# Kernel tuning notes

Measured on AMD Instinct MI355X. Metric: run time of the kernel, lower is better.

## Reference

```python
import math
import jax, jax.numpy as jnp
import numpy as np

B, N, DIM, H, DH = 2, 1024, 1024, 16, 64
SCALE = 16.0  # cosine_sim_scale
LN_EPS = 1e-5


def layer_norm(x, g, eps=LN_EPS):
    # torch: unbiased=False variance
    m = jnp.mean(x, axis=-1, keepdims=True)
    v = jnp.var(x, axis=-1, keepdims=True)
    return (x - m) * jax.lax.rsqrt(v + eps) * g


def l2norm(t):
    # F.normalize(dim=-1): x / max(||x||, 1e-12)
    n = jnp.linalg.norm(t, axis=-1, keepdims=True)
    return t / jnp.maximum(n, 1e-12)


def setup_inputs() -> dict:
    key = jax.random.key(0)
    ks = jax.random.split(key, 8)
    x = jax.random.normal(ks[0], (B, N, DIM), jnp.float32)
    attn_bias = jax.random.normal(ks[1], (B, H, N, N + 1), jnp.float32) * 0.02
    g_in = jnp.ones((DIM,), jnp.float32)
    w_q = jax.random.normal(ks[2], (H * DH, DIM), jnp.float32) * 0.02
    w_kv = jax.random.normal(ks[3], (2 * DH, DIM), jnp.float32) * 0.02
    null_kv = jax.random.normal(ks[4], (2, DH), jnp.float32)
    w_out = jax.random.normal(ks[5], (DIM, H * DH), jnp.float32) * 0.02
    g_out = jnp.ones((DIM,), jnp.float32)
    mask = jnp.ones((B, N), dtype=bool)
    return dict(x=x, attn_bias=attn_bias, g_in=g_in, w_q=w_q, w_kv=w_kv,
                null_kv=null_kv, w_out=w_out, g_out=g_out, mask=mask)


def reference(x, attn_bias, g_in, w_q, w_kv, null_kv, w_out, g_out, mask):
    b, n, _ = x.shape
    xn = layer_norm(x, g_in)
    q = xn @ w_q.T                      # [b, n, H*DH]
    kv = xn @ w_kv.T                    # [b, n, 2*DH]  (single kv head)
    k, v = kv[..., :DH], kv[..., DH:]
    q = q.reshape(b, n, H, DH).transpose(0, 2, 1, 3) * SCALE  # [b, h, n, d]
    nk = jnp.broadcast_to(null_kv[0], (b, 1, DH))
    nv = jnp.broadcast_to(null_kv[1], (b, 1, DH))
    k = jnp.concatenate([nk, k], axis=1)  # [b, n+1, d]
    v = jnp.concatenate([nv, v], axis=1)
    # cosine-sim attention: l2norm then scale by sqrt(cosine_sim_scale)
    q = l2norm(q) * math.sqrt(SCALE)
    k = l2norm(k) * math.sqrt(SCALE)
    sim = jnp.einsum('bhid,bjd->bhij', q, k) + attn_bias
    mask_p = jnp.concatenate([jnp.ones((b, 1), dtype=bool), mask], axis=1)  # null kv always visible
    max_neg = -jnp.finfo(sim.dtype).max
    sim = jnp.where(mask_p[:, None, None, :], sim, max_neg)
    attn = jax.nn.softmax(sim.astype(jnp.float32), axis=-1).astype(sim.dtype)
    out = jnp.einsum('bhij,bjd->bhid', attn, v)
    out = out.transpose(0, 2, 1, 3).reshape(b, n, H * DH)
    out = out @ w_out.T
    return layer_norm(out, g_out)
```

## Files before the change

kernel.cpp:

```cpp
#include <hip/hip_runtime.h>
#include <math.h>

#define B_   2
#define N_   1024
#define DIM_ 1024
#define H_   16
#define NK_  1025
#define NKP_ 1088
#define LOG2E 1.4426950408889634f

typedef __attribute__((ext_vector_type(8))) short s16x8;
typedef __attribute__((ext_vector_type(4))) float f32x4;

__device__ __forceinline__ float wave_sum(float v) {
  #pragma unroll
  for (int off = 32; off; off >>= 1) v += __shfl_xor(v, off);
  return v;
}
__device__ __forceinline__ short f2bf(float f) {
  union { float f; unsigned u; } v; v.f = f;
  unsigned r = (v.u + 0x7fffu + ((v.u >> 16) & 1u)) >> 16;
  return (short)r;
}
__device__ __forceinline__ float bf2f(short s) {
  union { unsigned u; float f; } v; v.u = ((unsigned)(unsigned short)s) << 16;
  return v.f;
}
__device__ __forceinline__ void gl_lds16(const void* g, void* lds) {
  __builtin_amdgcn_global_load_lds(
      (const __attribute__((address_space(1))) void*)g,
      (__attribute__((address_space(3))) void*)lds, 16, 0, 0);
}
__device__ __forceinline__ void gl_lds4(const void* g, void* lds) {
  __builtin_amdgcn_global_load_lds(
      (const __attribute__((address_space(1))) void*)g,
      (__attribute__((address_space(3))) void*)lds, 4, 0, 0);
}

__device__ __forceinline__ size_t kf_idx(int b, int j, int d) {
  return (((size_t)b * 68 + (j >> 4)) * 2 + (d >> 5)) * 512
         + (size_t)((((d >> 3) & 3) << 4) + (j & 15)) * 8 + (d & 7);
}
__device__ __forceinline__ size_t vf_idx(int b, int j, int d) {
  return (((size_t)b * 17 + (j >> 6)) * 8 + ((d >> 4) << 1) + ((j >> 5) & 1)) * 512
         + (size_t)((((j >> 3) & 3) << 4) + (d & 15)) * 8 + (j & 7);
}

__global__ __launch_bounds__(256) void pre_k(const float* __restrict__ wq,
                                             const float* __restrict__ wkv,
                                             const float* __restrict__ wout,
                                             short* __restrict__ Wqkv,
                                             short* __restrict__ Wout,
                                             const float* __restrict__ x,
                                             const float* __restrict__ g,
                                             short* __restrict__ xo,
                                             const float* __restrict__ nullkv,
                                             short* __restrict__ Kf,
                                             short* __restrict__ Vf) {
  if (blockIdx.x < 2176) {
    int i = (blockIdx.x * 256 + threadIdx.x) * 4;
    const float* s; short* d; int k;
    if (i < 1048576)      { s = wq;   d = Wqkv;           k = i; }
    else if (i < 1179648) { s = wkv;  d = Wqkv + 1048576; k = i - 1048576; }
    else                  { s = wout; d = Wout;           k = i - 1179648; }
    float4 v = *(const float4*)&s[k];
    short4 r; r.x = f2bf(v.x); r.y = f2bf(v.y); r.z = f2bf(v.z); r.w = f2bf(v.w);
    *(short4*)&d[k] = r;
    return;
  }
  if (blockIdx.x == 2176 + 2048) {
    int l = threadIdx.x & 63, w = threadIdx.x >> 6;
    if (w == 0) {
      float kk = nullkv[l];
      float n = sqrtf(wave_sum(kk * kk));
      short kv = f2bf(kk * (4.0f / fmaxf(n, 1e-12f)));
      Kf[kf_idx(0, 0, l)] = kv; Kf[kf_idx(1, 0, l)] = kv;
    } else if (w == 1) {
      short vv = f2bf(nullkv[64 + l]);
      Vf[vf_idx(0, 0, l)] = vv; Vf[vf_idx(1, 0, l)] = vv;
    } else if (w == 2) {
      for (int j = 1025; j < 1088; ++j) { Kf[kf_idx(0, j, l)] = 0; Kf[kf_idx(1, j, l)] = 0; }
    } else {
      for (int j = 1025; j < 1088; ++j) { Vf[vf_idx(0, j, l)] = 0; Vf[vf_idx(1, j, l)] = 0; }
    }
    return;
  }
  int row = blockIdx.x - 2176, tid = threadIdx.x;
  const float* xr = x + (size_t)row * DIM_;
  float4 v = *(const float4*)&xr[tid * 4];
  float s  = v.x + v.y + v.z + v.w;
  float sq = v.x*v.x + v.y*v.y + v.z*v.z + v.w*v.w;
  s = wave_sum(s); sq = wave_sum(sq);
  __shared__ float red[8];
  int w = tid >> 6, lane = tid & 63;
  if (lane == 0) { red[w] = s; red[4 + w] = sq; }
  __syncthreads();
  s  = red[0] + red[1] + red[2] + red[3];
  sq = red[4] + red[5] + red[6] + red[7];
  float mean = s * (1.0f / DIM_);
  float var  = sq * (1.0f / DIM_) - mean * mean;
  float inv  = rsqrtf(var + 1e-5f);
  float4 g4 = *(const float4*)&g[tid * 4];
  short4 r;
  r.x = f2bf((v.x - mean) * inv * g4.x);
  r.y = f2bf((v.y - mean) * inv * g4.y);
  r.z = f2bf((v.z - mean) * inv * g4.z);
  r.w = f2bf((v.w - mean) * inv * g4.w);
  *(short4*)&xo[(size_t)row * DIM_ + tid * 4] = r;
}

__global__ __launch_bounds__(256) void ln_out(const short* __restrict__ xb,
                                              const float* __restrict__ g,
                                              float* __restrict__ o) {
  int row = blockIdx.x, tid = threadIdx.x;
  const short* xr = xb + (size_t)row * DIM_;
  short4 s4 = *(const short4*)&xr[tid * 4];
  float v0 = bf2f(s4.x), v1 = bf2f(s4.y), v2 = bf2f(s4.z), v3 = bf2f(s4.w);
  float s  = v0 + v1 + v2 + v3;
  float sq = v0*v0 + v1*v1 + v2*v2 + v3*v3;
  s = wave_sum(s); sq = wave_sum(sq);
  __shared__ float red[8];
  int w = tid >> 6, lane = tid & 63;
  if (lane == 0) { red[w] = s; red[4 + w] = sq; }
  __syncthreads();
  s  = red[0] + red[1] + red[2] + red[3];
  sq = red[4] + red[5] + red[6] + red[7];
  float mean = s * (1.0f / DIM_);
  float var  = sq * (1.0f / DIM_) - mean * mean;
  float inv  = rsqrtf(var + 1e-5f);
  float4 g4 = *(const float4*)&g[tid * 4];
  float4 r;
  r.x = (v0 - mean) * inv * g4.x;
  r.y = (v1 - mean) * inv * g4.y;
  r.z = (v2 - mean) * inv * g4.z;
  r.w = (v3 - mean) * inv * g4.w;
  *(float4*)&o[(size_t)row * DIM_ + tid * 4] = r;
}

__global__ __launch_bounds__(256) void gemm_qkv(const short* __restrict__ A,
                                                const short* __restrict__ W,
                                                short* __restrict__ Qbh,
                                                short* __restrict__ Kf,
                                                short* __restrict__ Vf) {
  __shared__ short sb[2][24 * 512];
  int tid = threadIdx.x, l = tid & 63, w = tid >> 6;
  int li = l & 15, lg = l >> 4;
  int m0 = blockIdx.y * 64, n0 = blockIdx.x * 128;
  int wm = w & 1, wn = w >> 1;

  const short* src[6];
  #pragma unroll
  for (int s = 0; s < 6; ++s) {
    int c6 = w * 6 + s;
    if (c6 < 8) { int cm = c6 >> 1, ck = c6 & 1;
      src[s] = A + (size_t)(m0 + cm * 16 + li) * DIM_ + ck * 32 + lg * 8;
    } else { int cw = c6 - 8, cn = cw >> 1, ck = cw & 1;
      src[s] = W + (size_t)(n0 + cn * 16 + li) * DIM_ + ck * 32 + lg * 8;
    }
  }

  f32x4 acc[2][4];
  #pragma unroll
  for (int mi = 0; mi < 2; ++mi)
    #pragma unroll
    for (int ni = 0; ni < 4; ++ni) {
      acc[mi][ni][0] = 0.f; acc[mi][ni][1] = 0.f;
      acc[mi][ni][2] = 0.f; acc[mi][ni][3] = 0.f;
    }

  #pragma unroll
  for (int s = 0; s < 6; ++s) gl_lds16(src[s], &sb[0][(w * 6 + s) * 512]);
  __syncthreads();

  int cur = 0;
  for (int kt = 0; kt < 16; ++kt) {
    if (kt + 1 < 16) {
      #pragma unroll
      for (int s = 0; s < 6; ++s)
        gl_lds16(src[s] + (size_t)(kt + 1) * 64, &sb[cur ^ 1][(w * 6 + s) * 512]);
    }
    const short* sc = &sb[cur][0];
    #pragma unroll
    for (int ck = 0; ck < 2; ++ck) {
      s16x8 a0 = *(const s16x8*)&sc[((wm * 2 + 0) * 2 + ck) * 512 + l * 8];
      s16x8 a1 = *(const s16x8*)&sc[((wm * 2 + 1) * 2 + ck) * 512 + l * 8];
      #pragma unroll
      for (int ni = 0; ni < 4; ++ni) {
        s16x8 bf = *(const s16x8*)&sc[(8 + (wn * 4 + ni) * 2 + ck) * 512 + l * 8];
        acc[0][ni] = __builtin_amdgcn_mfma_f32_16x16x32_bf16(a0, bf, acc[0][ni], 0, 0, 0);
        acc[1][ni] = __builtin_amdgcn_mfma_f32_16x16x32_bf16(a1, bf, acc[1][ni], 0, 0, 0);
      }
    }
    __syncthreads();
    cur ^= 1;
  }

  bool isq = (blockIdx.x < 8);
  bool isk = (!isq) && (wn == 0);
  #pragma unroll
  for (int mi = 0; mi < 2; ++mi)
    #pragma unroll
    for (int rr = 0; rr < 4; ++rr) {
      int m = m0 + wm * 32 + mi * 16 + lg * 4 + rr;
      int b = m >> 10, i = m & 1023;
      float sc = 1.0f;
      if (isq || isk) {
        float ss = acc[mi][0][rr]*acc[mi][0][rr] + acc[mi][1][rr]*acc[mi][1][rr]
                 + acc[mi][2][rr]*acc[mi][2][rr] + acc[mi][3][rr]*acc[mi][3][rr];
        ss += __shfl_xor(ss, 1); ss += __shfl_xor(ss, 2);
        ss += __shfl_xor(ss, 4); ss += __shfl_xor(ss, 8);
        sc = 4.0f / fmaxf(sqrtf(ss), 1e-12f);
        if (isq) sc *= LOG2E;
      }
      if (isq) {
        int h = blockIdx.x * 2 + wn;
        #pragma unroll
        for (int ni = 0; ni < 4; ++ni)
          Qbh[(((size_t)(b * H_ + h)) * N_ + i) * 64 + ni * 16 + li] = f2bf(acc[mi][ni][rr] * sc);
      } else if (isk) {
        int j = i + 1;
        #pragma unroll
        for (int ni = 0; ni < 4; ++ni)
          Kf[kf_idx(b, j, ni * 16 + li)] = f2bf(acc[mi][ni][rr] * sc);
      } else {
        int j = i + 1;
        #pragma unroll
        for (int ni = 0; ni < 4; ++ni)
          Vf[vf_idx(b, j, ni * 16 + li)] = f2bf(acc[mi][ni][rr]);
      }
    }
}

__global__ __launch_bounds__(256) void gemm_bf(const short* __restrict__ A,
                                               const short* __restrict__ W,
                                               short* __restrict__ C,
                                               int M, int Nn, int K) {
  __shared__ short sb[2][24 * 512];
  int tid = threadIdx.x, l = tid & 63, w = tid >> 6;
  int li = l & 15, lg = l >> 4;
  int m0 = blockIdx.y * 64, n0 = blockIdx.x * 128;
  int wm = w & 1, wn = w >> 1;

  const short* src[6];
  #pragma unroll
  for (int s = 0; s < 6; ++s) {
    int c6 = w * 6 + s;
    if (c6 < 8) { int cm = c6 >> 1, ck = c6 & 1;
      src[s] = A + (size_t)(m0 + cm * 16 + li) * K + ck * 32 + lg * 8;
    } else { int cw = c6 - 8, cn = cw >> 1, ck = cw & 1;
      src[s] = W + (size_t)(n0 + cn * 16 + li) * K + ck * 32 + lg * 8;
    }
  }

  f32x4 acc[2][4];
  #pragma unroll
  for (int mi = 0; mi < 2; ++mi)
    #pragma unroll
    for (int ni = 0; ni < 4; ++ni) {
      acc[mi][ni][0] = 0.f; acc[mi][ni][1] = 0.f;
      acc[mi][ni][2] = 0.f; acc[mi][ni][3] = 0.f;
    }

  #pragma unroll
  for (int s = 0; s < 6; ++s) gl_lds16(src[s], &sb[0][(w * 6 + s) * 512]);
  __syncthreads();

  int KT = K >> 6, cur = 0;
  for (int kt = 0; kt < KT; ++kt) {
    if (kt + 1 < KT) {
      #pragma unroll
      for (int s = 0; s < 6; ++s)
        gl_lds16(src[s] + (size_t)(kt + 1) * 64, &sb[cur ^ 1][(w * 6 + s) * 512]);
    }
    const short* sc = &sb[cur][0];
    #pragma unroll
    for (int ck = 0; ck < 2; ++ck) {
      s16x8 a0 = *(const s16x8*)&sc[((wm * 2 + 0) * 2 + ck) * 512 + l * 8];
      s16x8 a1 = *(const s16x8*)&sc[((wm * 2 + 1) * 2 + ck) * 512 + l * 8];
      #pragma unroll
      for (int ni = 0; ni < 4; ++ni) {
        s16x8 bf = *(const s16x8*)&sc[(8 + (wn * 4 + ni) * 2 + ck) * 512 + l * 8];
        acc[0][ni] = __builtin_amdgcn_mfma_f32_16x16x32_bf16(a0, bf, acc[0][ni], 0, 0, 0);
        acc[1][ni] = __builtin_amdgcn_mfma_f32_16x16x32_bf16(a1, bf, acc[1][ni], 0, 0, 0);
      }
    }
    __syncthreads();
    cur ^= 1;
  }
  #pragma unroll
  for (int mi = 0; mi < 2; ++mi)
    #pragma unroll
    for (int ni = 0; ni < 4; ++ni)
      #pragma unroll
      for (int rr = 0; rr < 4; ++rr)
        C[(size_t)(m0 + wm * 32 + mi * 16 + lg * 4 + rr) * Nn
          + n0 + wn * 64 + ni * 16 + li] = f2bf(acc[mi][ni][rr]);
}

__global__ __launch_bounds__(256, 2) void attn_v10(const short* __restrict__ Qbh,
                                                   const short* __restrict__ Kf,
                                                   const short* __restrict__ Vf,
                                                   const float* __restrict__ bias,
                                                   short* __restrict__ O) {
  __shared__ float sBias[4][2][16][132];
  __shared__ short sP[4][1024];

  int tid = threadIdx.x, l = tid & 63, w = tid >> 6;
  int li = l & 15, lg = l >> 4;
  int bid = blockIdx.x;
  int it = bid & 15, h = (bid >> 4) & 15, b = bid >> 8;
  int i0 = it * 64 + w * 16;

  const short* qbase = Qbh + (((size_t)(b * H_ + h)) * N_ + i0 + li) * 64 + lg * 8;
  s16x8 qf0 = *(const s16x8*)qbase;
  s16x8 qf1 = *(const s16x8*)(qbase + 32);

  const short* kfb = Kf + (size_t)b * 68 * 2 * 512;
  const short* vfb = Vf + (size_t)b * 17 * 8 * 512;
  const float* brow = bias + ((size_t)(b * H_ + h) * N_ + i0) * NK_;

  auto stage_bias = [&](int g) {
    int buf = g & 1;
    #pragma unroll
    for (int r = 0; r < 16; ++r) {
      const float* src = brow + (size_t)r * NK_ + g * 128;
      float* dst = &sBias[w][buf][r][0];
      gl_lds4(src + l, dst);
      gl_lds4(src + 64 + l, dst + 64);
    }
  };
  auto load_k = [&](int jt, s16x8 (&kk)[8]) {
    #pragma unroll
    for (int c = 0; c < 8; ++c)
      kk[c] = *(const s16x8*)&kfb[((size_t)jt * 8 + c) * 512 + l * 8];
  };
  auto load_v = [&](int jt, s16x8 (&vv)[8]) {
    #pragma unroll
    for (int c = 0; c < 8; ++c)
      vv[c] = *(const s16x8*)&vfb[((size_t)jt * 8 + c) * 512 + l * 8];
  };

  s16x8 kl0 = *(const s16x8*)&kfb[((size_t)64 * 2 + 0) * 512 + lg * 128];
  s16x8 kl1 = *(const s16x8*)&kfb[((size_t)64 * 2 + 1) * 512 + lg * 128];
  float se = 0.f;
  #pragma unroll
  for (int e = 0; e < 8; ++e)
    se += bf2f(qf0[e]) * bf2f(kl0[e]) + bf2f(qf1[e]) * bf2f(kl1[e]);
  se += __shfl_xor(se, 16);
  se += __shfl_xor(se, 32);
  se = fmaf(bias[((size_t)(b * H_ + h) * N_ + i0 + li) * NK_ + 1024], LOG2E, se);

  float m_ = se, l_ = 1.f;
  f32x4 o[4];
  #pragma unroll
  for (int dt = 0; dt < 4; ++dt)
    #pragma unroll
    for (int rr = 0; rr < 4; ++rr)
      o[dt][rr] = bf2f(vfb[((size_t)16 * 8 + dt * 2) * 512 + (lg * 4 + rr) * 8]);

  short* pw = &sP[w][0];
  s16x8 kA[8], kB[8], vC[8];

  stage_bias(0);
  load_k(0, kA);
  __builtin_amdgcn_sched_barrier(0);

  auto compute = [&](int t, int g, s16x8 (&kC)[8]) {
    f32x4 st[4];
    #pragma unroll
    for (int jt4 = 0; jt4 < 4; ++jt4) {
      f32x4 cc; cc[0] = 0.f; cc[1] = 0.f; cc[2] = 0.f; cc[3] = 0.f;
      cc = __builtin_amdgcn_mfma_f32_16x16x32_bf16(kC[jt4 * 2 + 0], qf0, cc, 0, 0, 0);
      cc = __builtin_amdgcn_mfma_f32_16x16x32_bf16(kC[jt4 * 2 + 1], qf1, cc, 0, 0, 0);
      st[jt4] = cc;
    }
    int half = t & 1;
    float vmax = -1e30f;
    #pragma unroll
    for (int jt4 = 0; jt4 < 4; ++jt4) {
      f32x4 bb = *(const f32x4*)&sBias[w][g & 1][li][half * 64 + jt4 * 16 + lg * 4];
      #pragma unroll
      for (int rr = 0; rr < 4; ++rr) {
        st[jt4][rr] = fmaf(bb[rr], LOG2E, st[jt4][rr]);
        vmax = fmaxf(vmax, st[jt4][rr]);
      }
    }
    vmax = fmaxf(vmax, __shfl_xor(vmax, 16));
    vmax = fmaxf(vmax, __shfl_xor(vmax, 32));
    float mnew = fmaxf(m_, vmax);
    float cre = exp2f(m_ - mnew);
    m_ = mnew;
    float psum = 0.f;
    #pragma unroll
    for (int jt4 = 0; jt4 < 4; ++jt4)
      #pragma unroll
      for (int rr = 0; rr < 4; ++rr) {
        float pv = exp2f(st[jt4][rr] - mnew);
        st[jt4][rr] = pv;
        psum += pv;
      }
    psum += __shfl_xor(psum, 16);
    psum += __shfl_xor(psum, 32);
    l_ = l_ * cre + psum;
    #pragma unroll
    for (int dt = 0; dt < 4; ++dt) {
      o[dt][0] *= cre; o[dt][1] *= cre; o[dt][2] *= cre; o[dt][3] *= cre;
    }
    #pragma unroll
    for (int jt4 = 0; jt4 < 4; ++jt4) {
      int kfw = jt4 >> 1;
      int gw  = 2 * (jt4 & 1) + (lg >> 1);
      int ew  = (lg & 1) * 4;
      int off = kfw * 512 + (gw * 16 + li) * 8 + ew;
      #pragma unroll
      for (int rr = 0; rr < 4; ++rr) pw[off + rr] = f2bf(st[jt4][rr]);
    }
    s16x8 pb0 = *(const s16x8*)&pw[l * 8];
    s16x8 pb1 = *(const s16x8*)&pw[512 + l * 8];
    #pragma unroll
    for (int dt = 0; dt < 4; ++dt) {
      o[dt] = __builtin_amdgcn_mfma_f32_16x16x32_bf16(vC[dt * 2 + 0], pb0, o[dt], 0, 0, 0);
      o[dt] = __builtin_amdgcn_mfma_f32_16x16x32_bf16(vC[dt * 2 + 1], pb1, o[dt], 0, 0, 0);
    }
  };

  #pragma unroll
  for (int g = 0; g < 8; ++g) {
    {
      if (2 * g + 1 < 16) load_k(2 * g + 1, kB);
      load_v(2 * g, vC);
      __builtin_amdgcn_sched_barrier(0);
      compute(2 * g, g, kA);
    }
    {
      if (g + 1 < 8) stage_bias(g + 1);
      if (2 * g + 2 < 16) load_k(2 * g + 2, kA);
      load_v(2 * g + 1, vC);
      __builtin_amdgcn_sched_barrier(0);
      compute(2 * g + 1, g, kB);
    }
  }

  float inv = 1.f / l_;
  size_t obase = ((size_t)(b * N_ + i0 + li) * H_ + h) * 64;
  #pragma unroll
  for (int dt = 0; dt < 4; ++dt)
    #pragma unroll
    for (int rp = 0; rp < 2; ++rp) {
      unsigned lo = (unsigned short)f2bf(o[dt][rp * 2]     * inv);
      unsigned hi = (unsigned short)f2bf(o[dt][rp * 2 + 1] * inv);
      *(unsigned*)&O[obase + dt * 16 + lg * 4 + rp * 2] = lo | (hi << 16);
    }
}

extern "C" void kernel_launch(void* const* d_in, const int* in_sizes, int n_in,
                              void* d_out, int out_size, void* d_ws, size_t ws_size,
                              hipStream_t stream) {
  (void)in_sizes; (void)n_in; (void)out_size; (void)ws_size;
  const float* x       = (const float*)d_in[0];
  const float* bias    = (const float*)d_in[1];
  const float* g_in    = (const float*)d_in[2];
  const float* w_q     = (const float*)d_in[3];
  const float* w_kv    = (const float*)d_in[4];
  const float* null_kv = (const float*)d_in[5];
  const float* w_out   = (const float*)d_in[6];
  const float* g_out   = (const float*)d_in[7];

  char* p = (char*)d_ws;
  short* XNbf = (short*)p;
  short* Wqkv = (short*)(p + 4194304);
  short* Wout = (short*)(p + 6553600);
  short* Cout = (short*)(p + 8650752);
  short* Qbh  = (short*)(p + 12845056);
  short* Kf   = (short*)(p + 17039360);
  short* Vf   = (short*)(p + 17317888);
  short* AOUT = XNbf;
  float* out  = (float*)d_out;

  pre_k<<<2176 + 2048 + 1, 256, 0, stream>>>(w_q, w_kv, w_out, Wqkv, Wout,
                                             x, g_in, XNbf, null_kv, Kf, Vf);
  gemm_qkv<<<dim3(9, 32), 256, 0, stream>>>(XNbf, Wqkv, Qbh, Kf, Vf);
  attn_v10<<<B_ * H_ * (N_ / 64), 256, 0, stream>>>(Qbh, Kf, Vf, bias, AOUT);
  gemm_bf<<<dim3(8, 32), 256, 0, stream>>>(AOUT, Wout, Cout, B_ * N_, DIM_, DIM_);
  ln_out<<<B_ * N_, 256, 0, stream>>>(Cout, g_out, out);
}
```

Baseline: 98.15 us.

## Split attention KV range across waves with split-softmax combine per 16-row block

Each block now handles 16 query rows instead of 64, with its four waves each processing a quarter of the keys and merging partial max, sum and output through LDS at the end. The whole 16x1025 bias tile is loaded contiguously into LDS up front with direct global-to-LDS loads, replacing per-wave double-buffered staging. This gives four times as many blocks and more coalesced bias reads. In exchange it adds an up-front load stall, a block-wide reduction, larger LDS use that may limit occupancy, and less overlap between loads and compute.

```diff
diff --git a/kernel.cpp b/kernel.cpp
--- a/kernel.cpp
+++ b/kernel.cpp
@@ -68,7 +68,7 @@
     *(short4*)&d[k] = r;
     return;
   }
-  if (blockIdx.x == 2176 + 2048) {
+  if (blockIdx.x == 4224) {
     int l = threadIdx.x & 63, w = threadIdx.x >> 6;
     if (w == 0) {
       float kk = nullkv[l];
@@ -297,19 +297,19 @@
           + n0 + wn * 64 + ni * 16 + li] = f2bf(acc[mi][ni][rr]);
 }
 
-__global__ __launch_bounds__(256, 2) void attn_v10(const short* __restrict__ Qbh,
+__global__ __launch_bounds__(256, 2) void attn_v11(const short* __restrict__ Qbh,
                                                    const short* __restrict__ Kf,
                                                    const short* __restrict__ Vf,
                                                    const float* __restrict__ bias,
                                                    short* __restrict__ O) {
-  __shared__ float sBias[4][2][16][132];
+  __shared__ float sBias[16448];
   __shared__ short sP[4][1024];
 
   int tid = threadIdx.x, l = tid & 63, w = tid >> 6;
   int li = l & 15, lg = l >> 4;
   int bid = blockIdx.x;
-  int it = bid & 15, h = (bid >> 4) & 15, b = bid >> 8;
-  int i0 = it * 64 + w * 16;
+  int it = bid & 63, h = (bid >> 6) & 15, b = bid >> 10;
+  int i0 = it * 16;
 
   const short* qbase = Qbh + (((size_t)(b * H_ + h)) * N_ + i0 + li) * 64 + lg * 8;
   s16x8 qf0 = *(const s16x8*)qbase;
@@ -317,18 +317,20 @@
 
   const short* kfb = Kf + (size_t)b * 68 * 2 * 512;
   const short* vfb = Vf + (size_t)b * 17 * 8 * 512;
-  const float* brow = bias + ((size_t)(b * H_ + h) * N_ + i0) * NK_;
-
-  auto stage_bias = [&](int g) {
-    int buf = g & 1;
-    #pragma unroll
-    for (int r = 0; r < 16; ++r) {
-      const float* src = brow + (size_t)r * NK_ + g * 128;
-      float* dst = &sBias[w][buf][r][0];
-      gl_lds4(src + l, dst);
-      gl_lds4(src + 64 + l, dst + 64);
-    }
-  };
+  const float* ext = bias + ((size_t)(b * H_ + h) * N_ + i0) * NK_;
+
+  #pragma unroll 8
+  for (int k = 0; k < 64; ++k) {
+    int c = k * 4 + w;
+    gl_lds4(ext + c * 64 + l, &sBias[c * 64]);
+  }
+  if (w == 0) {
+    int idx = 16384 + l;
+    float v = 0.f;
+    if (idx < 16400) v = ext[idx];
+    sBias[idx] = v;
+  }
+
   auto load_k = [&](int jt, s16x8 (&kk)[8]) {
     #pragma unroll
     for (int c = 0; c < 8; ++c)
@@ -342,30 +344,40 @@
 
   s16x8 kl0 = *(const s16x8*)&kfb[((size_t)64 * 2 + 0) * 512 + lg * 128];
   s16x8 kl1 = *(const s16x8*)&kfb[((size_t)64 * 2 + 1) * 512 + lg * 128];
-  float se = 0.f;
-  #pragma unroll
-  for (int e = 0; e < 8; ++e)
-    se += bf2f(qf0[e]) * bf2f(kl0[e]) + bf2f(qf1[e]) * bf2f(kl1[e]);
-  se += __shfl_xor(se, 16);
-  se += __shfl_xor(se, 32);
-  se = fmaf(bias[((size_t)(b * H_ + h) * N_ + i0 + li) * NK_ + 1024], LOG2E, se);
-
-  float m_ = se, l_ = 1.f;
+
+  s16x8 kA[8], kB[8], vC[8];
+  int jt0 = w * 4;
+  load_k(jt0, kA);
+
+  __syncthreads();
+
+  float m_, l_;
   f32x4 o[4];
-  #pragma unroll
-  for (int dt = 0; dt < 4; ++dt)
-    #pragma unroll
-    for (int rr = 0; rr < 4; ++rr)
-      o[dt][rr] = bf2f(vfb[((size_t)16 * 8 + dt * 2) * 512 + (lg * 4 + rr) * 8]);
+  if (w == 0) {
+    float se = 0.f;
+    #pragma unroll
+    for (int e = 0; e < 8; ++e)
+      se += bf2f(qf0[e]) * bf2f(kl0[e]) + bf2f(qf1[e]) * bf2f(kl1[e]);
+    se += __shfl_xor(se, 16);
+    se += __shfl_xor(se, 32);
+    se = fmaf(sBias[li * 1025 + 1024], LOG2E, se);
+    m_ = se; l_ = 1.f;
+    #pragma unroll
+    for (int dt = 0; dt < 4; ++dt)
+      #pragma unroll
+      for (int rr = 0; rr < 4; ++rr)
+        o[dt][rr] = bf2f(vfb[((size_t)16 * 8 + dt * 2) * 512 + (lg * 4 + rr) * 8]);
+  } else {
+    m_ = -1e30f; l_ = 0.f;
+    #pragma unroll
+    for (int dt = 0; dt < 4; ++dt) {
+      o[dt][0] = 0.f; o[dt][1] = 0.f; o[dt][2] = 0.f; o[dt][3] = 0.f;
+    }
+  }
 
   short* pw = &sP[w][0];
-  s16x8 kA[8], kB[8], vC[8];
-
-  stage_bias(0);
-  load_k(0, kA);
-  __builtin_amdgcn_sched_barrier(0);
-
-  auto compute = [&](int t, int g, s16x8 (&kC)[8]) {
+
+  auto compute = [&](int jt, s16x8 (&kC)[8]) {
     f32x4 st[4];
     #pragma unroll
     for (int jt4 = 0; jt4 < 4; ++jt4) {
@@ -374,17 +386,15 @@
       cc = __builtin_amdgcn_mfma_f32_16x16x32_bf16(kC[jt4 * 2 + 1], qf1, cc, 0, 0, 0);
       st[jt4] = cc;
     }
-    int half = t & 1;
+    int bbase = li * 1025 + jt * 64 + lg * 4;
     float vmax = -1e30f;
     #pragma unroll
-    for (int jt4 = 0; jt4 < 4; ++jt4) {
-      f32x4 bb = *(const f32x4*)&sBias[w][g & 1][li][half * 64 + jt4 * 16 + lg * 4];
+    for (int jt4 = 0; jt4 < 4; ++jt4)
       #pragma unroll
       for (int rr = 0; rr < 4; ++rr) {
-        st[jt4][rr] = fmaf(bb[rr], LOG2E, st[jt4][rr]);
+        st[jt4][rr] = fmaf(sBias[bbase + jt4 * 16 + rr], LOG2E, st[jt4][rr]);
         vmax = fmaxf(vmax, st[jt4][rr]);
       }
-    }
     vmax = fmaxf(vmax, __shfl_xor(vmax, 16));
     vmax = fmaxf(vmax, __shfl_xor(vmax, 32));
     float mnew = fmaxf(m_, vmax);
@@ -424,33 +434,48 @@
     }
   };
 
-  #pragma unroll
-  for (int g = 0; g < 8; ++g) {
-    {
-      if (2 * g + 1 < 16) load_k(2 * g + 1, kB);
-      load_v(2 * g, vC);
-      __builtin_amdgcn_sched_barrier(0);
-      compute(2 * g, g, kA);
-    }
-    {
-      if (g + 1 < 8) stage_bias(g + 1);
-      if (2 * g + 2 < 16) load_k(2 * g + 2, kA);
-      load_v(2 * g + 1, vC);
-      __builtin_amdgcn_sched_barrier(0);
-      compute(2 * g + 1, g, kB);
-    }
-  }
-
-  float inv = 1.f / l_;
-  size_t obase = ((size_t)(b * N_ + i0 + li) * H_ + h) * 64;
+  load_k(jt0 + 1, kB);  load_v(jt0 + 0, vC);  compute(jt0 + 0, kA);
+  load_k(jt0 + 2, kA);  load_v(jt0 + 1, vC);  compute(jt0 + 1, kB);
+  load_k(jt0 + 3, kB);  load_v(jt0 + 2, vC);  compute(jt0 + 2, kA);
+                        load_v(jt0 + 3, vC);  compute(jt0 + 3, kB);
+
+  __syncthreads();
+  float* sM = sBias;
+  float* sL = sBias + 64;
+  float* sO = sBias + 128;
+  if (lg == 0) { sM[w * 16 + li] = m_; sL[w * 16 + li] = l_; }
   #pragma unroll
   for (int dt = 0; dt < 4; ++dt)
     #pragma unroll
-    for (int rp = 0; rp < 2; ++rp) {
-      unsigned lo = (unsigned short)f2bf(o[dt][rp * 2]     * inv);
-      unsigned hi = (unsigned short)f2bf(o[dt][rp * 2 + 1] * inv);
-      *(unsigned*)&O[obase + dt * 16 + lg * 4 + rp * 2] = lo | (hi << 16);
-    }
+    for (int rr = 0; rr < 4; ++rr)
+      sO[w * 1088 + (dt * 16 + lg * 4 + rr) * 17 + li] = o[dt][rr];
+  __syncthreads();
+
+  if (w == 0) {
+    float m0 = sM[li], m1 = sM[16 + li], m2 = sM[32 + li], m3 = sM[48 + li];
+    float mm = fmaxf(fmaxf(m0, m1), fmaxf(m2, m3));
+    float f0 = exp2f(m0 - mm), f1 = exp2f(m1 - mm);
+    float f2 = exp2f(m2 - mm), f3 = exp2f(m3 - mm);
+    float L = sL[li] * f0 + sL[16 + li] * f1 + sL[32 + li] * f2 + sL[48 + li] * f3;
+    float inv = 1.0f / L;
+    f0 *= inv; f1 *= inv; f2 *= inv; f3 *= inv;
+    size_t obase = ((size_t)(b * N_ + i0 + li) * H_ + h) * 64;
+    #pragma unroll
+    for (int dt = 0; dt < 4; ++dt)
+      #pragma unroll
+      for (int rp = 0; rp < 2; ++rp) {
+        float v0 = 0.f, v1 = 0.f;
+        int d0 = dt * 16 + lg * 4 + rp * 2;
+        v0 = sO[d0 * 17 + li] * f0 + sO[1088 + d0 * 17 + li] * f1
+           + sO[2176 + d0 * 17 + li] * f2 + sO[3264 + d0 * 17 + li] * f3;
+        int d1 = d0 + 1;
+        v1 = sO[d1 * 17 + li] * f0 + sO[1088 + d1 * 17 + li] * f1
+           + sO[2176 + d1 * 17 + li] * f2 + sO[3264 + d1 * 17 + li] * f3;
+        unsigned lo = (unsigned short)f2bf(v0);
+        unsigned hi = (unsigned short)f2bf(v1);
+        *(unsigned*)&O[obase + d0] = lo | (hi << 16);
+      }
+  }
 }
 
 extern "C" void kernel_launch(void* const* d_in, const int* in_sizes, int n_in,
@@ -480,7 +505,7 @@
   pre_k<<<2176 + 2048 + 1, 256, 0, stream>>>(w_q, w_kv, w_out, Wqkv, Wout,
                                              x, g_in, XNbf, null_kv, Kf, Vf);
   gemm_qkv<<<dim3(9, 32), 256, 0, stream>>>(XNbf, Wqkv, Qbh, Kf, Vf);
-  attn_v10<<<B_ * H_ * (N_ / 64), 256, 0, stream>>>(Qbh, Kf, Vf, bias, AOUT);
+  attn_v11<<<B_ * H_ * 64, 256, 0, stream>>>(Qbh, Kf, Vf, bias, AOUT);
   gemm_bf<<<dim3(8, 32), 256, 0, stream>>>(AOUT, Wout, Cout, B_ * N_, DIM_, DIM_);
   ln_out<<<B_ * N_, 256, 0, stream>>>(Cout, g_out, out);
 }
```

Result: slower. 106.5 us (+8.5%).
